# Kernel optimization log

Hardware: AMD Instinct MI355X
Metric: run time of the kernel (lower is better)

## Reference

```python
import jax, jax.numpy as jnp
import numpy as np

N = 100000      # nodes
R = 3           # relations (num_relations)
E = 200000      # edges per relation
F_IN = 128      # in_channels
HID = 128       # hidden_channels
OUT = 64        # out_channels
H = 4           # attention heads


def setup_inputs() -> dict:
    key = jax.random.key(0)
    ks = jax.random.split(key, 16)
    s = lambda d: np.float32(1.0 / np.sqrt(d))
    x = jax.random.normal(ks[0], (N, F_IN), jnp.float32)
    edge_index = jax.random.randint(ks[1], (R, 2, E), 0, N)
    dh1, dh2 = HID // H, OUT // H
    # layer 1 params (in=128 -> hid=128)
    Wk1 = jax.random.normal(ks[2], (F_IN, HID), jnp.float32) * s(F_IN)
    Wq1 = jax.random.normal(ks[3], (F_IN, HID), jnp.float32) * s(F_IN)
    Wv1 = jax.random.normal(ks[4], (F_IN, HID), jnp.float32) * s(F_IN)
    A1 = jax.random.normal(ks[5], (R, H, dh1, dh1), jnp.float32) * s(dh1)  # per-relation attention transform
    M1 = jax.random.normal(ks[6], (R, H, dh1, dh1), jnp.float32) * s(dh1)  # per-relation message transform
    prior1 = jnp.ones((R, H), jnp.float32)  # relation priors mu
    Wo1 = jax.random.normal(ks[7], (HID, HID), jnp.float32) * s(HID)
    # layer 2 params (hid=128 -> out=64)
    Wk2 = jax.random.normal(ks[8], (HID, OUT), jnp.float32) * s(HID)
    Wq2 = jax.random.normal(ks[9], (HID, OUT), jnp.float32) * s(HID)
    Wv2 = jax.random.normal(ks[10], (HID, OUT), jnp.float32) * s(HID)
    A2 = jax.random.normal(ks[11], (R, H, dh2, dh2), jnp.float32) * s(dh2)
    M2 = jax.random.normal(ks[12], (R, H, dh2, dh2), jnp.float32) * s(dh2)
    prior2 = jnp.ones((R, H), jnp.float32)
    Wo2 = jax.random.normal(ks[13], (OUT, OUT), jnp.float32) * s(OUT)
    return dict(x=x, edge_index=edge_index,
                Wk1=Wk1, Wq1=Wq1, Wv1=Wv1, A1=A1, M1=M1, prior1=prior1, Wo1=Wo1,
                Wk2=Wk2, Wq2=Wq2, Wv2=Wv2, A2=A2, M2=M2, prior2=prior2, Wo2=Wo2)


def _hgt_conv(x, edge_index, Wk, Wq, Wv, A, M, prior, Wo):
    """Heterogeneous graph transformer conv: per-relation K/Q/V attention,
    dst-grouped segment softmax, scatter-add aggregation, output projection."""
    n = x.shape[0]
    d_out = Wk.shape[1]
    heads = A.shape[1]
    dh = d_out // heads
    k = (x @ Wk).reshape(n, heads, dh)
    q = (x @ Wq).reshape(n, heads, dh)
    v = (x @ Wv).reshape(n, heads, dh)
    src = edge_index[:, 0, :]  # [R,E]
    dst = edge_index[:, 1, :]  # [R,E]
    # per-relation transformed keys / messages on edges
    k_e = jnp.einsum('rehd,rhdf->rehf', k[src], A)          # [R,E,H,dh]
    msg = jnp.einsum('rehd,rhdf->rehf', v[src], M)          # [R,E,H,dh]
    score = jnp.einsum('rehf,rehf->reh', k_e, q[dst])
    score = score * prior[:, None, :] * np.float32(1.0 / np.sqrt(dh))
    # flatten all relations for a joint softmax over each destination node
    e_tot = src.size
    dst_f = dst.reshape(e_tot)
    score = score.reshape(e_tot, heads)
    msg = msg.reshape(e_tot, heads, dh)
    smax = jax.ops.segment_max(score, dst_f, num_segments=n)
    smax = jnp.where(jnp.isfinite(smax), smax, 0.0)         # nodes with no in-edges
    ex = jnp.exp(score - smax[dst_f])
    denom = jax.ops.segment_sum(ex, dst_f, num_segments=n)
    alpha = ex / (denom[dst_f] + 1e-9)                      # [E_tot,H]
    aggr = jax.ops.segment_sum(msg * alpha[..., None], dst_f, num_segments=n)
    return aggr.reshape(n, d_out) @ Wo


def reference(x, edge_index, Wk1, Wq1, Wv1, A1, M1, prior1, Wo1,
              Wk2, Wq2, Wv2, A2, M2, prior2, Wo2):
    h = _hgt_conv(x, edge_index, Wk1, Wq1, Wv1, A1, M1, prior1, Wo1)
    h = jax.nn.relu(h)
    return _hgt_conv(h, edge_index, Wk2, Wq2, Wv2, A2, M2, prior2, Wo2)
```

## Files before the change

kernel.cpp:

```cpp
#include <hip/hip_runtime.h>

#define NN 100000
#define RR 3
#define EE 200000
#define HH 4
#define ETOT (RR * EE)
#define NB ((NN + 255) / 256)

typedef __attribute__((ext_vector_type(8))) short bf16x8;
typedef __attribute__((ext_vector_type(4))) float f32x4;

__device__ __forceinline__ int clampi(int v, int lo, int hi) {
  return v < lo ? lo : (v > hi ? hi : v);
}

__device__ __forceinline__ void split2(float v, ushort& h, ushort& l) {
  uint u = __float_as_uint(v);
  uint hb = (u + 0x7FFFu + ((u >> 16) & 1u)) >> 16;
  float fh = __uint_as_float(hb << 16);
  float r = v - fh;
  uint ur = __float_as_uint(r);
  uint lb = (ur + 0x7FFFu + ((ur >> 16) & 1u)) >> 16;
  h = (ushort)hb; l = (ushort)lb;
}

__device__ __forceinline__ ushort f2bf(float v) {
  uint u = __float_as_uint(v);
  return (ushort)((u + 0x7FFFu + ((u >> 16) & 1u)) >> 16);
}

__global__ __launch_bounds__(256) void to_bf16(
    const float* __restrict__ A, ushort* __restrict__ Ah, int total8)
{
  int idx = blockIdx.x * 256 + threadIdx.x;
  if (idx >= total8) return;
  const float4* ap = (const float4*)(A + (size_t)idx * 8);
  float4 a0 = ap[0], a1 = ap[1];
  const float v[8] = {a0.x, a0.y, a0.z, a0.w, a1.x, a1.y, a1.z, a1.w};
  ushort h[8];
  #pragma unroll
  for (int i = 0; i < 8; ++i) h[i] = f2bf(v[i]);
  *(uint4*)(Ah + (size_t)idx * 8) = *(const uint4*)h;
}

template<int KT>
__global__ __launch_bounds__(256) void gemm_bf1(
    const ushort* __restrict__ Ah, const ushort* __restrict__ Bth,
    int M, int NTOT,
    ushort* __restrict__ kb, int nk, ushort* __restrict__ vb,
    ushort* __restrict__ qb, int nq, int reluq)
{
  constexpr int K = KT * 32;
  constexpr int LDB = KT * 16 + 4;
  __shared__ uint Bs[2][64 * LDB];
  const int tid = threadIdx.x;
  const int m0 = blockIdx.x * 128;
  const int lane = tid & 63, wv = tid >> 6;
  const int rbase = m0 + wv * 32 + (lane & 15);
  const int kof = (lane >> 4) * 8;

  bf16x8 a[2][KT];
  #pragma unroll
  for (int m = 0; m < 2; ++m) {
    const int row = rbase + m * 16;
    #pragma unroll
    for (int kt = 0; kt < KT; ++kt) {
      uint4 u = make_uint4(0, 0, 0, 0);
      if (row < M) u = *(const uint4*)(Ah + (size_t)row * K + kt * 32 + kof);
      a[m][kt] = *reinterpret_cast<bf16x8*>(&u);
    }
  }

  auto stage = [&](int cb, int b) {
    const int c = tid >> 2, kq = tid & 3;
    if (kq * 32 < K) {
      const uint4* s = (const uint4*)(Bth + (size_t)(cb + c) * K + kq * 32);
      uint4* d = (uint4*)&Bs[b][c * LDB + kq * 16];
      #pragma unroll
      for (int q = 0; q < 4; ++q) d[q] = s[q];
    }
  };
  stage(0, 0);
  __syncthreads();
  int buf = 0;

  for (int cb = 0; cb < NTOT; cb += 64) {
    if (cb + 64 < NTOT) stage(cb + 64, buf ^ 1);

    f32x4 acc[2][4];
    #pragma unroll
    for (int m = 0; m < 2; ++m)
      #pragma unroll
      for (int n = 0; n < 4; ++n) acc[m][n] = (f32x4){0.f, 0.f, 0.f, 0.f};

    #pragma unroll
    for (int kt = 0; kt < KT; ++kt) {
      #pragma unroll
      for (int n = 0; n < 4; ++n) {
        const int boff = (n * 16 + (lane & 15)) * LDB + kt * 16 + (lane >> 4) * 4;
        uint4 u = *(const uint4*)&Bs[buf][boff];
        bf16x8 b8 = *reinterpret_cast<bf16x8*>(&u);
        acc[0][n] = __builtin_amdgcn_mfma_f32_16x16x32_bf16(a[0][kt], b8, acc[0][n], 0, 0, 0);
        acc[1][n] = __builtin_amdgcn_mfma_f32_16x16x32_bf16(a[1][kt], b8, acc[1][n], 0, 0, 0);
      }
    }

    ushort* ob; int stride, cbase, relu = 0;
    if (cb < nk)            { ob = kb; stride = nk; cbase = cb; }
    else if (cb < 2 * nk)   { ob = vb; stride = nk; cbase = cb - nk; }
    else                    { ob = qb; stride = nq; cbase = cb - 2 * nk; relu = reluq; }
    #pragma unroll
    for (int m = 0; m < 2; ++m) {
      const int rw = m0 + wv * 32 + m * 16 + (lane >> 4) * 4;
      #pragma unroll
      for (int n = 0; n < 4; ++n) {
        const int col = cbase + n * 16 + (lane & 15);
        #pragma unroll
        for (int j = 0; j < 4; ++j) {
          if (rw + j < M) {
            float o = acc[m][n][j];
            if (relu) o = fmaxf(o, 0.f);
            ob[(size_t)(rw + j) * stride + col] = f2bf(o);
          }
        }
      }
    }
    __syncthreads();
    buf ^= 1;
  }
}

template<int KT>
__global__ __launch_bounds__(256) void gemm_sp3(
    const ushort* __restrict__ Ah, const ushort* __restrict__ Al,
    const ushort* __restrict__ Bth, const ushort* __restrict__ Btl,
    int M, int NTOT, float* __restrict__ of)
{
  constexpr int K = KT * 32;
  constexpr int LDB = KT * 16 + 4;
  __shared__ uint Bh[64 * LDB];
  __shared__ uint Bl[64 * LDB];
  const int tid = threadIdx.x;
  const int m0 = blockIdx.x * 128;
  const int lane = tid & 63, wv = tid >> 6;
  const int rbase = m0 + wv * 32 + (lane & 15);
  const int kof = (lane >> 4) * 8;

  bf16x8 ah[2][KT], al[2][KT];
  #pragma unroll
  for (int m = 0; m < 2; ++m) {
    const int row = rbase + m * 16;
    #pragma unroll
    for (int kt = 0; kt < KT; ++kt) {
      uint4 uh = make_uint4(0, 0, 0, 0), ul = make_uint4(0, 0, 0, 0);
      if (row < M) {
        uh = *(const uint4*)(Ah + (size_t)row * K + kt * 32 + kof);
        ul = *(const uint4*)(Al + (size_t)row * K + kt * 32 + kof);
      }
      ah[m][kt] = *reinterpret_cast<bf16x8*>(&uh);
      al[m][kt] = *reinterpret_cast<bf16x8*>(&ul);
    }
  }

  for (int cb = 0; cb < NTOT; cb += 64) {
    {
      const int c = tid >> 2, kq = tid & 3;
      if (kq * 32 < K) {
        const uint4* sh = (const uint4*)(Bth + (size_t)(cb + c) * K + kq * 32);
        const uint4* sl = (const uint4*)(Btl + (size_t)(cb + c) * K + kq * 32);
        uint4* dh = (uint4*)&Bh[c * LDB + kq * 16];
        uint4* dl = (uint4*)&Bl[c * LDB + kq * 16];
        #pragma unroll
        for (int q = 0; q < 4; ++q) { dh[q] = sh[q]; dl[q] = sl[q]; }
      }
    }
    __syncthreads();

    f32x4 acc[2][4];
    #pragma unroll
    for (int m = 0; m < 2; ++m)
      #pragma unroll
      for (int n = 0; n < 4; ++n) acc[m][n] = (f32x4){0.f, 0.f, 0.f, 0.f};

    #pragma unroll
    for (int kt = 0; kt < KT; ++kt) {
      #pragma unroll
      for (int n = 0; n < 4; ++n) {
        const int boff = (n * 16 + (lane & 15)) * LDB + kt * 16 + (lane >> 4) * 4;
        uint4 uh = *(const uint4*)&Bh[boff];
        uint4 ul = *(const uint4*)&Bl[boff];
        bf16x8 bh = *reinterpret_cast<bf16x8*>(&uh);
        bf16x8 bl = *reinterpret_cast<bf16x8*>(&ul);
        #pragma unroll
        for (int m = 0; m < 2; ++m) {
          acc[m][n] = __builtin_amdgcn_mfma_f32_16x16x32_bf16(ah[m][kt], bh, acc[m][n], 0, 0, 0);
          acc[m][n] = __builtin_amdgcn_mfma_f32_16x16x32_bf16(ah[m][kt], bl, acc[m][n], 0, 0, 0);
          acc[m][n] = __builtin_amdgcn_mfma_f32_16x16x32_bf16(al[m][kt], bh, acc[m][n], 0, 0, 0);
        }
      }
    }

    #pragma unroll
    for (int m = 0; m < 2; ++m) {
      const int rw = m0 + wv * 32 + m * 16 + (lane >> 4) * 4;
      #pragma unroll
      for (int n = 0; n < 4; ++n) {
        const int col = cb + n * 16 + (lane & 15);
        #pragma unroll
        for (int j = 0; j < 4; ++j)
          if (rw + j < M) of[(size_t)(rw + j) * NTOT + col] = acc[m][n][j];
      }
    }
    __syncthreads();
  }
}

__global__ __launch_bounds__(256) void convt(
    const float* __restrict__ W, ushort* __restrict__ Th, ushort* __restrict__ Tl,
    int K, int N)
{
  int idx = blockIdx.x * 256 + threadIdx.x;
  if (idx >= K * N) return;
  int n = idx / K, k = idx % K;
  ushort h, l; split2(W[(size_t)k * N + n], h, l);
  Th[(size_t)n * K + k] = h;
  Tl[(size_t)n * K + k] = l;
}

__global__ __launch_bounds__(256) void build_wT(
    const float* __restrict__ W, const float* __restrict__ T,
    ushort* __restrict__ Oh, ushort* __restrict__ Ol, int F, int D, int dh)
{
  const int cols = RR * D;
  int idx = blockIdx.x * 256 + threadIdx.x;
  if (idx >= F * cols) return;
  int i = idx / cols, c = idx % cols;
  int r = c / D, gf = c % D;
  int h = gf / dh, f = gf % dh;
  const float* w = W + (size_t)i * D + h * dh;
  const float* t = T + ((size_t)(r * HH + h) * dh) * dh + f;
  float s = 0.f;
  for (int d = 0; d < dh; ++d) s = fmaf(w[d], t[(size_t)d * dh], s);
  ushort hh, ll; split2(s, hh, ll);
  Oh[(size_t)c * F + i] = hh;
  Ol[(size_t)c * F + i] = ll;
}

__global__ __launch_bounds__(256) void zero_i32(int* __restrict__ p, int n)
{
  int i = blockIdx.x * 256 + threadIdx.x;
  if (i < n) p[i] = 0;
}

__global__ __launch_bounds__(256) void csr_count(
    const int* __restrict__ EI, int* __restrict__ cnt)
{
  int idx = blockIdx.x * 256 + threadIdx.x;
  if (idx >= ETOT) return;
  int r = idx / EE, e = idx % EE;
  int dst = clampi(EI[(size_t)r * 2 * EE + EE + e], 0, NN - 1);
  atomicAdd(&cnt[dst], 1);
}

__global__ __launch_bounds__(256) void scan_intra(
    int* __restrict__ arr, int* __restrict__ blksum)
{
  __shared__ int s[256];
  const int t = threadIdx.x;
  const int i = blockIdx.x * 256 + t;
  int v = (i < NN) ? arr[i] : 0;
  s[t] = v;
  __syncthreads();
  #pragma unroll
  for (int off = 1; off < 256; off <<= 1) {
    int x = (t >= off) ? s[t - off] : 0;
    __syncthreads();
    s[t] += x;
    __syncthreads();
  }
  if (i < NN) arr[i] = s[t] - v;
  if (t == 255) blksum[blockIdx.x] = s[255];
}

__global__ __launch_bounds__(256) void scan_mid(
    const int* __restrict__ blksum, int* __restrict__ blkoff)
{
  __shared__ int s[256];
  __shared__ int carry;
  const int t = threadIdx.x;
  if (t == 0) carry = 0;
  __syncthreads();
  for (int base = 0; base < NB; base += 256) {
    const int i = base + t;
    int v = (i < NB) ? blksum[i] : 0;
    s[t] = v;
    __syncthreads();
    #pragma unroll
    for (int off = 1; off < 256; off <<= 1) {
      int x = (t >= off) ? s[t - off] : 0;
      __syncthreads();
      s[t] += x;
      __syncthreads();
    }
    if (i < NB) blkoff[i] = carry + s[t] - v;
    __syncthreads();
    if (t == 255) carry += s[255];
    __syncthreads();
  }
}

__global__ __launch_bounds__(256) void scan_add(
    int* __restrict__ arr, const int* __restrict__ blkoff,
    int* __restrict__ rowptr, int* __restrict__ cursor)
{
  int i = blockIdx.x * 256 + threadIdx.x;
  if (i < NN) {
    int v = arr[i] + blkoff[i >> 8];
    rowptr[i] = v;
    cursor[i] = v;
  }
  if (i == NN) rowptr[NN] = ETOT;
}

__global__ __launch_bounds__(256) void csr_scatter(
    const int* __restrict__ EI, int* __restrict__ cursor,
    int* __restrict__ srcrel)
{
  int idx = blockIdx.x * 256 + threadIdx.x;
  if (idx >= ETOT) return;
  int r = idx / EE, e = idx % EE;
  int src = clampi(EI[(size_t)r * 2 * EE + e], 0, NN - 1);
  int dst = clampi(EI[(size_t)r * 2 * EE + EE + e], 0, NN - 1);
  int pos = atomicAdd(&cursor[dst], 1);
  pos = clampi(pos, 0, ETOT - 1);
  srcrel[pos] = src | (r << 24);
}

template<int D, int DH>
__global__ __launch_bounds__(256) void node_fused(
    const ushort* __restrict__ kb, const ushort* __restrict__ vb,
    const ushort* __restrict__ qb,
    const int* __restrict__ rowptr, const int* __restrict__ srcrel,
    const float* __restrict__ prior,
    ushort* __restrict__ agh, ushort* __restrict__ agl)
{
  constexpr int LPN = D / 2;
  constexpr int NPW = 64 / LPN;
  constexpr int SUB = DH / 2;
  const int lane = threadIdx.x & 63;
  const int wv = blockIdx.x * 4 + (threadIdx.x >> 6);
  const int n = wv * NPW + lane / LPN;
  const int sl = lane % LPN;
  if (n >= NN) return;
  const int h = sl / SUB;
  constexpr float scale = (DH == 32) ? 0.17677669529663687f : 0.25f;
  float pr[RR];
  #pragma unroll
  for (int r = 0; r < RR; ++r) pr[r] = prior[r * HH + h] * scale;
  const uint qu = *(const uint*)&qb[(size_t)n * D + sl * 2];
  const float qx = __uint_as_float(qu << 16);
  const float qy = __uint_as_float(qu & 0xFFFF0000u);
  const int j0 = clampi(rowptr[n], 0, ETOT);
  const int j1 = clampi(rowptr[n + 1], j0, ETOT);
  float2 acc = make_float2(0.f, 0.f);
  float den = 0.f;
  int j = j0;
  for (; j + 1 < j1; j += 2) {
    const int w0 = srcrel[j];
    const int w1 = srcrel[j + 1];
    const int s0i = clampi(w0 & 0xFFFFFF, 0, NN - 1);
    const int r0  = clampi(w0 >> 24, 0, RR - 1);
    const int s1i = clampi(w1 & 0xFFFFFF, 0, NN - 1);
    const int r1  = clampi(w1 >> 24, 0, RR - 1);
    const size_t b0 = (size_t)s0i * (RR * D) + r0 * D + sl * 2;
    const size_t b1 = (size_t)s1i * (RR * D) + r1 * D + sl * 2;
    const uint ku0 = *(const uint*)&kb[b0];
    const uint vu0 = *(const uint*)&vb[b0];
    const uint ku1 = *(const uint*)&kb[b1];
    const uint vu1 = *(const uint*)&vb[b1];
    float s0 = __uint_as_float(ku0 << 16) * qx + __uint_as_float(ku0 & 0xFFFF0000u) * qy;
    float s1 = __uint_as_float(ku1 << 16) * qx + __uint_as_float(ku1 & 0xFFFF0000u) * qy;
    #pragma unroll
    for (int off = SUB / 2; off >= 1; off >>= 1) {
      s0 += __shfl_xor(s0, off, 64);
      s1 += __shfl_xor(s1, off, 64);
    }
    const float ex0 = __expf(s0 * pr[r0]);
    const float ex1 = __expf(s1 * pr[r1]);
    den += ex0 + ex1;
    acc.x = fmaf(ex0, __uint_as_float(vu0 << 16), acc.x);
    acc.y = fmaf(ex0, __uint_as_float(vu0 & 0xFFFF0000u), acc.y);
    acc.x = fmaf(ex1, __uint_as_float(vu1 << 16), acc.x);
    acc.y = fmaf(ex1, __uint_as_float(vu1 & 0xFFFF0000u), acc.y);
  }
  if (j < j1) {
    const int w0 = srcrel[j];
    const int s0i = clampi(w0 & 0xFFFFFF, 0, NN - 1);
    const int r0  = clampi(w0 >> 24, 0, RR - 1);
    const size_t b0 = (size_t)s0i * (RR * D) + r0 * D + sl * 2;
    const uint ku0 = *(const uint*)&kb[b0];
    const uint vu0 = *(const uint*)&vb[b0];
    float s0 = __uint_as_float(ku0 << 16) * qx + __uint_as_float(ku0 & 0xFFFF0000u) * qy;
    #pragma unroll
    for (int off = SUB / 2; off >= 1; off >>= 1) s0 += __shfl_xor(s0, off, 64);
    const float ex0 = __expf(s0 * pr[r0]);
    den += ex0;
    acc.x = fmaf(ex0, __uint_as_float(vu0 << 16), acc.x);
    acc.y = fmaf(ex0, __uint_as_float(vu0 & 0xFFFF0000u), acc.y);
  }
  const float inv = 1.f / (den + 1e-9f);
  const float ox = acc.x * inv, oy = acc.y * inv;
  if (agl) {
    ushort h0, l0, h1, l1;
    split2(ox, h0, l0); split2(oy, h1, l1);
    *(uint*)&agh[(size_t)n * D + sl * 2] = (uint)h0 | ((uint)h1 << 16);
    *(uint*)&agl[(size_t)n * D + sl * 2] = (uint)l0 | ((uint)l1 << 16);
  } else {
    *(uint*)&agh[(size_t)n * D + sl * 2] = (uint)f2bf(ox) | ((uint)f2bf(oy) << 16);
  }
}

extern "C" void kernel_launch(void* const* d_in, const int* in_sizes, int n_in,
                              void* d_out, int out_size, void* d_ws, size_t ws_size,
                              hipStream_t stream)
{
  const float* x   = (const float*)d_in[0];
  const int*   EI  = (const int*)  d_in[1];
  const float* Wk1 = (const float*)d_in[2];
  const float* Wq1 = (const float*)d_in[3];
  const float* Wv1 = (const float*)d_in[4];
  const float* A1  = (const float*)d_in[5];
  const float* M1  = (const float*)d_in[6];
  const float* P1  = (const float*)d_in[7];
  const float* Wo1 = (const float*)d_in[8];
  const float* Wk2 = (const float*)d_in[9];
  const float* Wq2 = (const float*)d_in[10];
  const float* Wv2 = (const float*)d_in[11];
  const float* A2  = (const float*)d_in[12];
  const float* M2  = (const float*)d_in[13];
  const float* P2  = (const float*)d_in[14];
  const float* Wo2 = (const float*)d_in[15];
  float* out = (float*)d_out;

  float* ws = (float*)d_ws;
  const size_t nd = (size_t)NN * 128;
  ushort* xh   = (ushort*)ws;
  ushort* agh  = xh;
  ushort* qb2  = (ushort*)ws;
  ushort* ag2h = (ushort*)(ws + nd / 4);
  ushort* qb1  = (ushort*)(ws + nd / 2);
  ushort* ag2l = (ushort*)(ws + nd / 2);
  ushort* kb   = (ushort*)(ws + nd);
  ushort* vb   = (ushort*)(ws + 5 * nd / 2);
  ushort* Hbh  = (ushort*)(ws + 4 * nd);
  ushort* WBth = (ushort*)(ws + 5 * nd);
  ushort* WBtl = WBth + 896 * 128;
  int* ints   = (int*)(WBtl + 896 * 128);
  int* rowptr = ints;
  int* cursor = rowptr + NN + 1;
  int* blks   = cursor + NN;
  int* srcrel = blks + 2 * NB;

  const size_t need_bytes = (5 * nd + 114688) * 4 +
      ((size_t)(NN + 1) + NN + 2 * NB + ETOT) * 4;
  if (ws_size < need_bytes) return;

  dim3 blk(256);
  const int GB = (NN + 127) / 128;

  to_bf16<<<dim3((NN * 128 / 8 + 255) / 256), blk, 0, stream>>>(x, xh, NN * 128 / 8);
  build_wT<<<dim3(192), blk, 0, stream>>>(Wk1, A1, WBth, WBtl, 128, 128, 32);
  build_wT<<<dim3(192), blk, 0, stream>>>(Wv1, M1, WBth + 384 * 128, WBtl + 384 * 128, 128, 128, 32);
  convt<<<dim3(64), blk, 0, stream>>>(Wq1, WBth + 768 * 128, WBtl + 768 * 128, 128, 128);

  gemm_bf1<4><<<dim3(GB), blk, 0, stream>>>(xh, WBth, NN, 896, kb, 384, vb, qb1, 128, 0);

  zero_i32<<<dim3(NB), blk, 0, stream>>>(cursor, NN);
  csr_count<<<dim3((ETOT + 255) / 256), blk, 0, stream>>>(EI, cursor);
  scan_intra<<<dim3(NB), blk, 0, stream>>>(cursor, blks);
  scan_mid<<<dim3(1), blk, 0, stream>>>(blks, blks + NB);
  scan_add<<<dim3(NB), blk, 0, stream>>>(cursor, blks + NB, rowptr, cursor);
  csr_scatter<<<dim3((ETOT + 255) / 256), blk, 0, stream>>>(EI, cursor, srcrel);

  node_fused<128, 32><<<dim3((NN + 3) / 4), blk, 0, stream>>>(
      kb, vb, qb1, rowptr, srcrel, P1, agh, (ushort*)nullptr);
  convt<<<dim3(64), blk, 0, stream>>>(Wo1, WBth, WBtl, 128, 128);
  gemm_bf1<4><<<dim3(GB), blk, 0, stream>>>(agh, WBth, NN, 128,
                                            (ushort*)nullptr, 0, (ushort*)nullptr,
                                            Hbh, 128, 1);

  build_wT<<<dim3(96), blk, 0, stream>>>(Wk2, A2, WBth, WBtl, 128, 64, 16);
  build_wT<<<dim3(96), blk, 0, stream>>>(Wv2, M2, WBth + 192 * 128, WBtl + 192 * 128, 128, 64, 16);
  convt<<<dim3(32), blk, 0, stream>>>(Wq2, WBth + 384 * 128, WBtl + 384 * 128, 128, 64);
  gemm_bf1<4><<<dim3(GB), blk, 0, stream>>>(Hbh, WBth, NN, 448, kb, 192, vb, qb2, 64, 0);

  node_fused<64, 16><<<dim3((NN + 7) / 8), blk, 0, stream>>>(
      kb, vb, qb2, rowptr, srcrel, P2, ag2h, ag2l);
  convt<<<dim3(16), blk, 0, stream>>>(Wo2, WBth, WBtl, 64, 64);
  gemm_sp3<2><<<dim3(GB), blk, 0, stream>>>(ag2h, ag2l, WBth, WBtl, NN, 64, out);
}
```

Baseline: 350.7 us.

## Process multiple edges per wave in node aggregation and fold prior scaling into K weights

The edge-aggregation kernel now assigns one node per wavefront and splits the wave into slots that each handle a different incoming edge, with each lane loading four bf16 features instead of two. Partial sums are combined with a cross-slot shuffle reduction at the end. This exposes more memory-level parallelism for the irregular gathers, which matters because the average in-degree is only about six. The per-relation prior and the 1/sqrt(dh) scale are folded into the precomputed K weights, removing a multiply and a prior lookup per edge. In exchange, low-degree nodes leave slots idle, layer 2 no longer packs several nodes into one wave, and every lane pays for the final reduction.

```diff
diff --git a/kernel.cpp b/kernel.cpp
--- a/kernel.cpp
+++ b/kernel.cpp
@@ -229,7 +229,8 @@
 
 __global__ __launch_bounds__(256) void build_wT(
     const float* __restrict__ W, const float* __restrict__ T,
-    ushort* __restrict__ Oh, ushort* __restrict__ Ol, int F, int D, int dh)
+    ushort* __restrict__ Oh, ushort* __restrict__ Ol, int F, int D, int dh,
+    const float* __restrict__ prior, float scale)
 {
   const int cols = RR * D;
   int idx = blockIdx.x * 256 + threadIdx.x;
@@ -241,6 +242,7 @@
   const float* t = T + ((size_t)(r * HH + h) * dh) * dh + f;
   float s = 0.f;
   for (int d = 0; d < dh; ++d) s = fmaf(w[d], t[(size_t)d * dh], s);
+  if (prior) s *= prior[r * HH + h] * scale;
   ushort hh, ll; split2(s, hh, ll);
   Oh[(size_t)c * F + i] = hh;
   Ol[(size_t)c * F + i] = ll;
@@ -341,82 +343,75 @@
     const ushort* __restrict__ kb, const ushort* __restrict__ vb,
     const ushort* __restrict__ qb,
     const int* __restrict__ rowptr, const int* __restrict__ srcrel,
-    const float* __restrict__ prior,
     ushort* __restrict__ agh, ushort* __restrict__ agl)
 {
-  constexpr int LPN = D / 2;
-  constexpr int NPW = 64 / LPN;
-  constexpr int SUB = DH / 2;
+  constexpr int LPS = D / 4;
+  constexpr int ES  = 64 / LPS;
+  constexpr int SUB = DH / 4;
   const int lane = threadIdx.x & 63;
-  const int wv = blockIdx.x * 4 + (threadIdx.x >> 6);
-  const int n = wv * NPW + lane / LPN;
-  const int sl = lane % LPN;
+  const int wv = threadIdx.x >> 6;
+  const int n = blockIdx.x * 4 + wv;
   if (n >= NN) return;
-  const int h = sl / SUB;
-  constexpr float scale = (DH == 32) ? 0.17677669529663687f : 0.25f;
-  float pr[RR];
-  #pragma unroll
-  for (int r = 0; r < RR; ++r) pr[r] = prior[r * HH + h] * scale;
-  const uint qu = *(const uint*)&qb[(size_t)n * D + sl * 2];
-  const float qx = __uint_as_float(qu << 16);
-  const float qy = __uint_as_float(qu & 0xFFFF0000u);
+  const int slot = lane / LPS;
+  const int sl   = lane % LPS;
+  const uint2 qu = *(const uint2*)&qb[(size_t)n * D + sl * 4];
+  const float q0 = __uint_as_float(qu.x << 16);
+  const float q1 = __uint_as_float(qu.x & 0xFFFF0000u);
+  const float q2 = __uint_as_float(qu.y << 16);
+  const float q3 = __uint_as_float(qu.y & 0xFFFF0000u);
   const int j0 = clampi(rowptr[n], 0, ETOT);
   const int j1 = clampi(rowptr[n + 1], j0, ETOT);
-  float2 acc = make_float2(0.f, 0.f);
-  float den = 0.f;
-  int j = j0;
-  for (; j + 1 < j1; j += 2) {
-    const int w0 = srcrel[j];
-    const int w1 = srcrel[j + 1];
-    const int s0i = clampi(w0 & 0xFFFFFF, 0, NN - 1);
-    const int r0  = clampi(w0 >> 24, 0, RR - 1);
-    const int s1i = clampi(w1 & 0xFFFFFF, 0, NN - 1);
-    const int r1  = clampi(w1 >> 24, 0, RR - 1);
-    const size_t b0 = (size_t)s0i * (RR * D) + r0 * D + sl * 2;
-    const size_t b1 = (size_t)s1i * (RR * D) + r1 * D + sl * 2;
-    const uint ku0 = *(const uint*)&kb[b0];
-    const uint vu0 = *(const uint*)&vb[b0];
-    const uint ku1 = *(const uint*)&kb[b1];
-    const uint vu1 = *(const uint*)&vb[b1];
-    float s0 = __uint_as_float(ku0 << 16) * qx + __uint_as_float(ku0 & 0xFFFF0000u) * qy;
-    float s1 = __uint_as_float(ku1 << 16) * qx + __uint_as_float(ku1 & 0xFFFF0000u) * qy;
-    #pragma unroll
-    for (int off = SUB / 2; off >= 1; off >>= 1) {
-      s0 += __shfl_xor(s0, off, 64);
-      s1 += __shfl_xor(s1, off, 64);
-    }
-    const float ex0 = __expf(s0 * pr[r0]);
-    const float ex1 = __expf(s1 * pr[r1]);
-    den += ex0 + ex1;
-    acc.x = fmaf(ex0, __uint_as_float(vu0 << 16), acc.x);
-    acc.y = fmaf(ex0, __uint_as_float(vu0 & 0xFFFF0000u), acc.y);
-    acc.x = fmaf(ex1, __uint_as_float(vu1 << 16), acc.x);
-    acc.y = fmaf(ex1, __uint_as_float(vu1 & 0xFFFF0000u), acc.y);
-  }
-  if (j < j1) {
-    const int w0 = srcrel[j];
-    const int s0i = clampi(w0 & 0xFFFFFF, 0, NN - 1);
-    const int r0  = clampi(w0 >> 24, 0, RR - 1);
-    const size_t b0 = (size_t)s0i * (RR * D) + r0 * D + sl * 2;
-    const uint ku0 = *(const uint*)&kb[b0];
-    const uint vu0 = *(const uint*)&vb[b0];
-    float s0 = __uint_as_float(ku0 << 16) * qx + __uint_as_float(ku0 & 0xFFFF0000u) * qy;
-    #pragma unroll
-    for (int off = SUB / 2; off >= 1; off >>= 1) s0 += __shfl_xor(s0, off, 64);
-    const float ex0 = __expf(s0 * pr[r0]);
-    den += ex0;
-    acc.x = fmaf(ex0, __uint_as_float(vu0 << 16), acc.x);
-    acc.y = fmaf(ex0, __uint_as_float(vu0 & 0xFFFF0000u), acc.y);
-  }
-  const float inv = 1.f / (den + 1e-9f);
-  const float ox = acc.x * inv, oy = acc.y * inv;
-  if (agl) {
-    ushort h0, l0, h1, l1;
-    split2(ox, h0, l0); split2(oy, h1, l1);
-    *(uint*)&agh[(size_t)n * D + sl * 2] = (uint)h0 | ((uint)h1 << 16);
-    *(uint*)&agl[(size_t)n * D + sl * 2] = (uint)l0 | ((uint)l1 << 16);
-  } else {
-    *(uint*)&agh[(size_t)n * D + sl * 2] = (uint)f2bf(ox) | ((uint)f2bf(oy) << 16);
+  float a0 = 0.f, a1 = 0.f, a2 = 0.f, a3 = 0.f, den = 0.f;
+
+  for (int jb = j0; jb < j1; jb += ES) {
+    const int j = jb + slot;
+    const bool valid = j < j1;
+    const int jj = clampi(valid ? j : j0, 0, ETOT - 1);
+    const int w = srcrel[jj];
+    const int si = clampi(w & 0xFFFFFF, 0, NN - 1);
+    const int r  = clampi(w >> 24, 0, RR - 1);
+    const size_t base = (size_t)si * (RR * D) + r * D + sl * 4;
+    const uint2 ku = *(const uint2*)&kb[base];
+    const uint2 vu = *(const uint2*)&vb[base];
+    float s =        __uint_as_float(ku.x << 16)          * q0;
+    s = fmaf(__uint_as_float(ku.x & 0xFFFF0000u), q1, s);
+    s = fmaf(__uint_as_float(ku.y << 16),         q2, s);
+    s = fmaf(__uint_as_float(ku.y & 0xFFFF0000u), q3, s);
+    #pragma unroll
+    for (int off = SUB / 2; off >= 1; off >>= 1) s += __shfl_xor(s, off, 64);
+    const float ex = valid ? __expf(s) : 0.f;
+    den += ex;
+    a0 = fmaf(ex, __uint_as_float(vu.x << 16),          a0);
+    a1 = fmaf(ex, __uint_as_float(vu.x & 0xFFFF0000u),  a1);
+    a2 = fmaf(ex, __uint_as_float(vu.y << 16),          a2);
+    a3 = fmaf(ex, __uint_as_float(vu.y & 0xFFFF0000u),  a3);
+  }
+
+  #pragma unroll
+  for (int off = LPS; off < 64; off <<= 1) {
+    den += __shfl_xor(den, off, 64);
+    a0 += __shfl_xor(a0, off, 64);
+    a1 += __shfl_xor(a1, off, 64);
+    a2 += __shfl_xor(a2, off, 64);
+    a3 += __shfl_xor(a3, off, 64);
+  }
+
+  if (slot == 0) {
+    const float inv = 1.f / (den + 1e-9f);
+    const float o0 = a0 * inv, o1 = a1 * inv, o2 = a2 * inv, o3 = a3 * inv;
+    if (agl) {
+      ushort h0, l0, h1, l1, h2, l2, h3, l3;
+      split2(o0, h0, l0); split2(o1, h1, l1);
+      split2(o2, h2, l2); split2(o3, h3, l3);
+      uint2 ho = make_uint2((uint)h0 | ((uint)h1 << 16), (uint)h2 | ((uint)h3 << 16));
+      uint2 lo = make_uint2((uint)l0 | ((uint)l1 << 16), (uint)l2 | ((uint)l3 << 16));
+      *(uint2*)&agh[(size_t)n * D + sl * 4] = ho;
+      *(uint2*)&agl[(size_t)n * D + sl * 4] = lo;
+    } else {
+      uint2 ho = make_uint2((uint)f2bf(o0) | ((uint)f2bf(o1) << 16),
+                            (uint)f2bf(o2) | ((uint)f2bf(o3) << 16));
+      *(uint2*)&agh[(size_t)n * D + sl * 4] = ho;
+    }
   }
 }
 
@@ -467,10 +462,13 @@
 
   dim3 blk(256);
   const int GB = (NN + 127) / 128;
+  const int NFB = (NN + 3) / 4;
 
   to_bf16<<<dim3((NN * 128 / 8 + 255) / 256), blk, 0, stream>>>(x, xh, NN * 128 / 8);
-  build_wT<<<dim3(192), blk, 0, stream>>>(Wk1, A1, WBth, WBtl, 128, 128, 32);
-  build_wT<<<dim3(192), blk, 0, stream>>>(Wv1, M1, WBth + 384 * 128, WBtl + 384 * 128, 128, 128, 32);
+  build_wT<<<dim3(192), blk, 0, stream>>>(Wk1, A1, WBth, WBtl, 128, 128, 32,
+                                          P1, 0.17677669529663687f);
+  build_wT<<<dim3(192), blk, 0, stream>>>(Wv1, M1, WBth + 384 * 128, WBtl + 384 * 128,
+                                          128, 128, 32, (const float*)nullptr, 1.f);
   convt<<<dim3(64), blk, 0, stream>>>(Wq1, WBth + 768 * 128, WBtl + 768 * 128, 128, 128);
 
   gemm_bf1<4><<<dim3(GB), blk, 0, stream>>>(xh, WBth, NN, 896, kb, 384, vb, qb1, 128, 0);
@@ -482,20 +480,22 @@
   scan_add<<<dim3(NB), blk, 0, stream>>>(cursor, blks + NB, rowptr, cursor);
   csr_scatter<<<dim3((ETOT + 255) / 256), blk, 0, stream>>>(EI, cursor, srcrel);
 
-  node_fused<128, 32><<<dim3((NN + 3) / 4), blk, 0, stream>>>(
-      kb, vb, qb1, rowptr, srcrel, P1, agh, (ushort*)nullptr);
+  node_fused<128, 32><<<dim3(NFB), blk, 0, stream>>>(
+      kb, vb, qb1, rowptr, srcrel, agh, (ushort*)nullptr);
   convt<<<dim3(64), blk, 0, stream>>>(Wo1, WBth, WBtl, 128, 128);
   gemm_bf1<4><<<dim3(GB), blk, 0, stream>>>(agh, WBth, NN, 128,
                                             (ushort*)nullptr, 0, (ushort*)nullptr,
                                             Hbh, 128, 1);
 
-  build_wT<<<dim3(96), blk, 0, stream>>>(Wk2, A2, WBth, WBtl, 128, 64, 16);
-  build_wT<<<dim3(96), blk, 0, stream>>>(Wv2, M2, WBth + 192 * 128, WBtl + 192 * 128, 128, 64, 16);
+  build_wT<<<dim3(96), blk, 0, stream>>>(Wk2, A2, WBth, WBtl, 128, 64, 16,
+                                         P2, 0.25f);
+  build_wT<<<dim3(96), blk, 0, stream>>>(Wv2, M2, WBth + 192 * 128, WBtl + 192 * 128,
+                                         128, 64, 16, (const float*)nullptr, 1.f);
   convt<<<dim3(32), blk, 0, stream>>>(Wq2, WBth + 384 * 128, WBtl + 384 * 128, 128, 64);
   gemm_bf1<4><<<dim3(GB), blk, 0, stream>>>(Hbh, WBth, NN, 448, kb, 192, vb, qb2, 64, 0);
 
-  node_fused<64, 16><<<dim3((NN + 7) / 8), blk, 0, stream>>>(
-      kb, vb, qb2, rowptr, srcrel, P2, ag2h, ag2l);
+  node_fused<64, 16><<<dim3(NFB), blk, 0, stream>>>(
+      kb, vb, qb2, rowptr, srcrel, ag2h, ag2l);
   convt<<<dim3(16), blk, 0, stream>>>(Wo2, WBth, WBtl, 64, 64);
   gemm_sp3<2><<<dim3(GB), blk, 0, stream>>>(ag2h, ag2l, WBth, WBtl, NN, 64, out);
 }
```

Result: slower. 363.6 us (+3.7%).
